# Optimization experiments

Hardware: AMD Instinct MI355X
Metric: run time of the kernel (lower is better)

## Reference

```python
import jax, jax.numpy as jnp
import numpy as np

B, L, C, NH = 4, 2048, 512, 8
HD = C // NH  # head_dim = 64


def setup_inputs() -> dict:
    key = jax.random.key(0)
    k1, k2, k3, k4 = jax.random.split(key, 4)
    s = 1.0 / np.sqrt(C)
    return {
        "x": jax.random.normal(k1, (B, L, C), dtype=jnp.float32),
        "w_qkv": jax.random.normal(k2, (C, 3 * C), dtype=jnp.float32) * s,
        "b_qkv": jnp.zeros((3 * C,), dtype=jnp.float32),  # zeroed in __init__
        "w_proj": jax.random.normal(k3, (C, C), dtype=jnp.float32) * s,
        "b_proj": jax.random.normal(k4, (C,), dtype=jnp.float32) * 0.01,
    }


def reference(x, w_qkv, b_qkv, w_proj, b_proj):
    Bx, Lx, Cx = x.shape
    qkv = x @ w_qkv + b_qkv                       # [B, L, 3C]
    qkv = qkv.reshape(Bx, Lx, 3, NH, HD)          # 'B L (K H D)'
    qkv = jnp.transpose(qkv, (2, 0, 3, 1, 4))     # 'K B H L D'
    q, k, v = qkv[0], qkv[1], qkv[2]
    scale = 1.0 / np.sqrt(HD)
    scores = jnp.einsum('bhld,bhmd->bhlm', q, k) * scale  # [B, H, L, L]
    attn = jax.nn.softmax(scores, axis=-1)
    out = jnp.einsum('bhlm,bhmd->bhld', attn, v)  # [B, H, L, D]
    out = jnp.transpose(out, (0, 2, 1, 3)).reshape(Bx, Lx, Cx)  # 'B H L D -> B L (H D)'
    return out @ w_proj + b_proj
```

## Files before the change

kernel.cpp:

```cpp
#include <hip/hip_runtime.h>

#define B_   4
#define L_   2048
#define C_   512
#define NH_  8
#define HD_  64
#define M_   (B_ * L_)
#define N_QKV 1536

typedef __bf16 bf16x8 __attribute__((ext_vector_type(8)));
typedef float floatx4 __attribute__((ext_vector_type(4)));
typedef unsigned short ushort_t;

__device__ __forceinline__ unsigned pk2(float a, float b) {
  union { float f; unsigned u; } x, y;
  x.f = a; y.f = b;
  return __builtin_amdgcn_perm(y.u + 0x8000u, x.u + 0x8000u, 0x07060302u);
}

__device__ __forceinline__ ushort_t bf16h(float a) {
  union { float f; unsigned u; } x;
  x.f = a;
  return (ushort_t)((x.u + 0x8000u) >> 16);
}

__device__ __forceinline__ floatx4 mfma16(bf16x8 a, bf16x8 b, floatx4 c) {
  return __builtin_amdgcn_mfma_f32_16x16x32_bf16(a, b, c, 0, 0, 0);
}

__device__ __forceinline__ void gld_lds16(const void* g, void* s) {
  __builtin_amdgcn_global_load_lds(
      (const __attribute__((address_space(1))) unsigned int*)(g),
      (__attribute__((address_space(3))) unsigned int*)(s), 16, 0, 0);
}

__global__ __launch_bounds__(256) void convert_all_kernel(
    const float* __restrict__ x, const float* __restrict__ wq,
    const float* __restrict__ wp, ushort_t* __restrict__ xb,
    ushort_t* __restrict__ wqT, ushort_t* __restrict__ wpT) {
  __shared__ ushort_t tile[64][68];
  const int t = threadIdx.x;
  const int bid = blockIdx.x;
  if (bid < 2048) {
    size_t i = ((size_t)bid * 256 + t) * 8;
    float4 a = *(const float4*)(x + i);
    float4 b = *(const float4*)(x + i + 4);
    uint4 o;
    o.x = pk2(a.x, a.y);
    o.y = pk2(a.z, a.w);
    o.z = pk2(b.x, b.y);
    o.w = pk2(b.z, b.w);
    *(uint4*)(xb + i) = o;
    return;
  }
  const float* w;
  ushort_t* wt;
  int N, n0, k0;
  if (bid < 2240) {
    int b2 = bid - 2048;
    w = wq; wt = wqT; N = N_QKV;
    n0 = (b2 % 24) * 64; k0 = (b2 / 24) * 64;
  } else {
    int b2 = bid - 2240;
    w = wp; wt = wpT; N = C_;
    n0 = (b2 & 7) * 64; k0 = (b2 >> 3) * 64;
  }
  const int r = t >> 4, c4 = (t & 15) * 4;
#pragma unroll
  for (int i = 0; i < 4; ++i) {
    int k = r + i * 16;
    float4 v = *(const float4*)(w + (size_t)(k0 + k) * N + n0 + c4);
    uint2 p;
    p.x = pk2(v.x, v.y);
    p.y = pk2(v.z, v.w);
    *(uint2*)&tile[k][c4] = p;
  }
  __syncthreads();
#pragma unroll
  for (int i = 0; i < 4; ++i) {
    int n = r + i * 16;
    uint2 o;
    o.x = (unsigned)tile[c4 + 0][n] | ((unsigned)tile[c4 + 1][n] << 16);
    o.y = (unsigned)tile[c4 + 2][n] | ((unsigned)tile[c4 + 3][n] << 16);
    *(uint2*)(wt + (size_t)(n0 + n) * 512 + k0 + c4) = o;
  }
}

__global__ __launch_bounds__(256) void qkv_mfma_kernel(
    const ushort_t* __restrict__ A,
    const ushort_t* __restrict__ Bt,
    const float* __restrict__ bias,
    ushort_t* __restrict__ Qd, ushort_t* __restrict__ Kd,
    ushort_t* __restrict__ Vd) {
  __shared__ ushort_t As[2][4096];
  __shared__ ushort_t Bs[2][4096];

  const int t = threadIdx.x;
  const int w = t >> 6, l = t & 63;
  const int li = l & 15, lq = l >> 4;
  const int wm = w & 1, wn = w >> 1;
  const int m0 = blockIdx.x * 128;
  const int n0 = blockIdx.y * 128;

  const int inner = (l & 7) ^ (l >> 3);
  const int srow = (l >> 3) * 2 + (inner >> 2);
  const int skb = inner & 3;

  const ushort_t* asrc0 = A + (size_t)(m0 + (2 * w) * 16 + srow) * 512 + skb * 8;
  const ushort_t* asrc1 = A + (size_t)(m0 + (2 * w + 1) * 16 + srow) * 512 + skb * 8;
  const ushort_t* bsrc0 = Bt + (size_t)(n0 + (2 * w) * 16 + srow) * 512 + skb * 8;
  const ushort_t* bsrc1 = Bt + (size_t)(n0 + (2 * w + 1) * 16 + srow) * 512 + skb * 8;
  const int qo0 = (2 * w) * 512, qo1 = (2 * w + 1) * 512;

  const int foff = (li >> 1) * 128 + ((((li & 1) * 4 + lq)) ^ (li >> 1)) * 16;

  const floatx4 fz = {0.f, 0.f, 0.f, 0.f};
  floatx4 acc[4][4];
#pragma unroll
  for (int i = 0; i < 4; ++i)
#pragma unroll
    for (int j = 0; j < 4; ++j) acc[i][j] = fz;

  for (int kk = 0; kk < 8; ++kk) {
    __syncthreads();
#pragma unroll
    for (int kh = 0; kh < 2; ++kh) {
      gld_lds16(asrc0 + kh * 32, &As[kh][qo0]);
      gld_lds16(asrc1 + kh * 32, &As[kh][qo1]);
      gld_lds16(bsrc0 + kh * 32, &Bs[kh][qo0]);
      gld_lds16(bsrc1 + kh * 32, &Bs[kh][qo1]);
    }
    asrc0 += 64; asrc1 += 64; bsrc0 += 64; bsrc1 += 64;
    __syncthreads();

#pragma unroll
    for (int kh = 0; kh < 2; ++kh) {
      bf16x8 af[4], bfr[4];
#pragma unroll
      for (int mt = 0; mt < 4; ++mt)
        af[mt] = *(const bf16x8*)((const char*)&As[kh][0] +
                                  (wm * 64 + mt * 16) * 64 + foff);
#pragma unroll
      for (int nt = 0; nt < 4; ++nt)
        bfr[nt] = *(const bf16x8*)((const char*)&Bs[kh][0] +
                                   (wn * 64 + nt * 16) * 64 + foff);
#pragma unroll
      for (int mt = 0; mt < 4; ++mt)
#pragma unroll
        for (int nt = 0; nt < 4; ++nt)
          acc[mt][nt] = mfma16(af[mt], bfr[nt], acc[mt][nt]);
    }
  }

  const int n0g = n0 + wn * 64;
  const int kk2 = n0g >> 9, h = (n0g >> 6) & 7;
  const int mb = m0 + wm * 64;
  const int b = mb >> 11;
  const int bh = b * NH_ + h;
  const float SCQ = 0.18033688011f;
  float bb[4];
#pragma unroll
  for (int nt = 0; nt < 4; ++nt) bb[nt] = bias[n0g + nt * 16 + li];

  if (kk2 == 0) {
#pragma unroll
    for (int mt = 0; mt < 4; ++mt) {
      int lrow = (mb + mt * 16 + lq * 4) & (L_ - 1);
#pragma unroll
      for (int nt = 0; nt < 4; ++nt) {
        int d = nt * 16 + li;
        ushort_t* p = Qd + ((size_t)bh * L_ + lrow) * HD_ + d;
#pragma unroll
        for (int r = 0; r < 4; ++r)
          p[(size_t)r * HD_] = bf16h((acc[mt][nt][r] + bb[nt]) * SCQ);
      }
    }
  } else if (kk2 == 1) {
#pragma unroll
    for (int mt = 0; mt < 4; ++mt) {
      int lrow = (mb + mt * 16 + lq * 4) & (L_ - 1);
#pragma unroll
      for (int nt = 0; nt < 4; ++nt) {
        int d = nt * 16 + li;
        ushort_t* p = Kd + ((size_t)bh * L_ + lrow) * HD_ + d;
#pragma unroll
        for (int r = 0; r < 4; ++r)
          p[(size_t)r * HD_] = bf16h(acc[mt][nt][r] + bb[nt]);
      }
    }
  } else {
#pragma unroll
    for (int mt = 0; mt < 4; ++mt) {
      int tb = mb + mt * 16 + lq * 4;
      int c = (tb >> 6) & 31;
      int sp = (mt >> 1) & 1;
      int rem = tb & 31;
      int lq2 = rem >> 3;
      int h8 = (rem >> 2) & 1;
#pragma unroll
      for (int nt = 0; nt < 4; ++nt) {
        size_t off = ((size_t)(bh * 32 + c) * 512 +
                      ((sp * 4 + nt) * 4 + lq2) * 16 + li) * 8 + h8 * 4;
        uint2 v;
        v.x = pk2(acc[mt][nt][0] + bb[nt], acc[mt][nt][1] + bb[nt]);
        v.y = pk2(acc[mt][nt][2] + bb[nt], acc[mt][nt][3] + bb[nt]);
        *(uint2*)(Vd + off) = v;
      }
    }
  }
}

__global__ __launch_bounds__(256) void attn_kernel(
    const ushort_t* __restrict__ Qg, const ushort_t* __restrict__ Kg,
    const ushort_t* __restrict__ Vb, ushort_t* __restrict__ AO) {
  __shared__ ushort_t Ks[4][4096];
  __shared__ ushort_t Vs[4][4096];

  const int t = threadIdx.x;
  const int w = t >> 6, l = t & 63;
  const int li = l & 15, lq = l >> 4;
  const int bh = blockIdx.y;
  const int m0 = blockIdx.x * 128;

  const ushort_t* ksrc[2];
  const ushort_t* vsrc[2];
  int qoff[2];
#pragma unroll
  for (int u = 0; u < 2; ++u) {
    int q = 2 * w + u;
    int p = q * 64 + l;
    int key = p >> 3, pb = p & 7;
    int swz = (key & 3) | (((key >> 3) & 1) << 2);
    ksrc[u] = Kg + ((size_t)bh * L_ + key) * HD_ + (pb ^ swz) * 8;
    vsrc[u] = Vb + ((size_t)bh * 32 * 512 + p) * 8;
    qoff[u] = p * 8 & 4095;
  }

  bf16x8 qf[2][2];
#pragma unroll
  for (int g = 0; g < 2; ++g)
#pragma unroll
    for (int s = 0; s < 2; ++s)
      qf[g][s] = *(const bf16x8*)(Qg +
          ((size_t)bh * L_ + m0 + (2 * w + g) * 16 + li) * HD_ + 32 * s + lq * 8);

  const floatx4 fz = {0.f, 0.f, 0.f, 0.f};
  floatx4 O[2][4];
  float lsum[2] = {0.f, 0.f};
#pragma unroll
  for (int g = 0; g < 2; ++g)
#pragma unroll
    for (int dt = 0; dt < 4; ++dt) O[g][dt] = fz;

  const int keybase = 8 * (li >> 2) + (li & 3);
  const int xsw = li & 7;

  for (int c = 0; c < L_ / 256; ++c) {
    __syncthreads();
#pragma unroll
    for (int j = 0; j < 4; ++j) {
      gld_lds16(ksrc[0] + j * 4096, &Ks[j][qoff[0]]);
      gld_lds16(ksrc[1] + j * 4096, &Ks[j][qoff[1]]);
      gld_lds16(vsrc[0] + j * 4096, &Vs[j][qoff[0]]);
      gld_lds16(vsrc[1] + j * 4096, &Vs[j][qoff[1]]);
    }
    ksrc[0] += 16384; ksrc[1] += 16384;
    vsrc[0] += 16384; vsrc[1] += 16384;
    __syncthreads();

#pragma unroll
    for (int j = 0; j < 4; ++j) {
#pragma unroll
      for (int sp = 0; sp < 2; ++sp) {
        floatx4 sa[2][2];
#pragma unroll
        for (int g = 0; g < 2; ++g)
#pragma unroll
          for (int k2 = 0; k2 < 2; ++k2) sa[g][k2] = fz;

#pragma unroll
        for (int k2 = 0; k2 < 2; ++k2) {
          const char* rowb =
              (const char*)&Ks[j][0] + (32 * sp + 4 * k2 + keybase) * 128;
#pragma unroll
          for (int s = 0; s < 2; ++s) {
            bf16x8 kf = *(const bf16x8*)(rowb + ((4 * s + lq) ^ xsw) * 16);
            sa[0][k2] = mfma16(kf, qf[0][s], sa[0][k2]);
            sa[1][k2] = mfma16(kf, qf[1][s], sa[1][k2]);
          }
        }

        bf16x8 pf[2];
#pragma unroll
        for (int g = 0; g < 2; ++g) {
          float pv[2][4];
#pragma unroll
          for (int k2 = 0; k2 < 2; ++k2)
#pragma unroll
            for (int r = 0; r < 4; ++r) {
              float e = __builtin_amdgcn_exp2f(sa[g][k2][r]);
              pv[k2][r] = e;
              lsum[g] += e;
            }
          uint4 pk;
          pk.x = pk2(pv[0][0], pv[0][1]);
          pk.y = pk2(pv[0][2], pv[0][3]);
          pk.z = pk2(pv[1][0], pv[1][1]);
          pk.w = pk2(pv[1][2], pv[1][3]);
          pf[g] = __builtin_bit_cast(bf16x8, pk);
        }

#pragma unroll
        for (int dt = 0; dt < 4; ++dt) {
          bf16x8 vf = *(const bf16x8*)((const char*)&Vs[j][0] +
              sp * 4096 + dt * 1024 + lq * 256 + li * 16);
          O[0][dt] = mfma16(vf, pf[0], O[0][dt]);
          O[1][dt] = mfma16(vf, pf[1], O[1][dt]);
        }
      }
    }
  }

  const int b = bh >> 3, h = bh & 7;
#pragma unroll
  for (int g = 0; g < 2; ++g) {
    float s = lsum[g];
    s += __shfl_xor(s, 16, 64);
    s += __shfl_xor(s, 32, 64);
    float inv = 1.0f / s;
    int qrow = m0 + (2 * w + g) * 16 + li;
    ushort_t* base = AO + ((size_t)(b * L_ + qrow)) * C_ + h * HD_ + 4 * lq;
#pragma unroll
    for (int dt = 0; dt < 4; ++dt) {
      uint2 v;
      v.x = pk2(O[g][dt][0] * inv, O[g][dt][1] * inv);
      v.y = pk2(O[g][dt][2] * inv, O[g][dt][3] * inv);
      *(uint2*)(base + 16 * dt) = v;
    }
  }
}

__global__ __launch_bounds__(256) void proj_mfma_kernel(
    const ushort_t* __restrict__ A,
    const ushort_t* __restrict__ Bt,
    const float* __restrict__ bias, float* __restrict__ out) {
  __shared__ ushort_t As[2][2048];
  __shared__ ushort_t Bs[2][4096];

  const int t = threadIdx.x;
  const int w = t >> 6, l = t & 63;
  const int li = l & 15, lq = l >> 4;
  const int wm = w & 1, wn = w >> 1;
  const int m0 = blockIdx.x * 64;
  const int n0 = blockIdx.y * 128;

  const int inner = (l & 7) ^ (l >> 3);
  const int srow = (l >> 3) * 2 + (inner >> 2);
  const int skb = inner & 3;

  const ushort_t* asrc0 = A + (size_t)(m0 + w * 16 + srow) * 512 + skb * 8;
  const ushort_t* bsrc0 = Bt + (size_t)(n0 + (2 * w) * 16 + srow) * 512 + skb * 8;
  const ushort_t* bsrc1 = Bt + (size_t)(n0 + (2 * w + 1) * 16 + srow) * 512 + skb * 8;
  const int ao = w * 512;
  const int qo0 = (2 * w) * 512, qo1 = (2 * w + 1) * 512;

  const int foff = (li >> 1) * 128 + ((((li & 1) * 4 + lq)) ^ (li >> 1)) * 16;

  const floatx4 fz = {0.f, 0.f, 0.f, 0.f};
  floatx4 acc[2][4];
#pragma unroll
  for (int i = 0; i < 2; ++i)
#pragma unroll
    for (int j = 0; j < 4; ++j) acc[i][j] = fz;

  for (int kk = 0; kk < 8; ++kk) {
    __syncthreads();
#pragma unroll
    for (int kh = 0; kh < 2; ++kh) {
      gld_lds16(asrc0 + kh * 32, &As[kh][ao]);
      gld_lds16(bsrc0 + kh * 32, &Bs[kh][qo0]);
      gld_lds16(bsrc1 + kh * 32, &Bs[kh][qo1]);
    }
    asrc0 += 64; bsrc0 += 64; bsrc1 += 64;
    __syncthreads();

#pragma unroll
    for (int kh = 0; kh < 2; ++kh) {
      bf16x8 af[2], bfr[4];
#pragma unroll
      for (int mt = 0; mt < 2; ++mt)
        af[mt] = *(const bf16x8*)((const char*)&As[kh][0] +
                                  (wm * 32 + mt * 16) * 64 + foff);
#pragma unroll
      for (int nt = 0; nt < 4; ++nt)
        bfr[nt] = *(const bf16x8*)((const char*)&Bs[kh][0] +
                                   (wn * 64 + nt * 16) * 64 + foff);
#pragma unroll
      for (int mt = 0; mt < 2; ++mt)
#pragma unroll
        for (int nt = 0; nt < 4; ++nt)
          acc[mt][nt] = mfma16(af[mt], bfr[nt], acc[mt][nt]);
    }
  }

#pragma unroll
  for (int mt = 0; mt < 2; ++mt) {
    int m = m0 + wm * 32 + mt * 16 + lq * 4;
#pragma unroll
    for (int nt = 0; nt < 4; ++nt) {
      int n = n0 + wn * 64 + nt * 16 + li;
      float bb = bias[n];
#pragma unroll
      for (int r = 0; r < 4; ++r)
        out[(size_t)(m + r) * C_ + n] = acc[mt][nt][r] + bb;
    }
  }
}

extern "C" void kernel_launch(void* const* d_in, const int* in_sizes, int n_in,
                              void* d_out, int out_size, void* d_ws,
                              size_t ws_size, hipStream_t stream) {
  const float* x      = (const float*)d_in[0];
  const float* w_qkv  = (const float*)d_in[1];
  const float* b_qkv  = (const float*)d_in[2];
  const float* w_proj = (const float*)d_in[3];
  const float* b_proj = (const float*)d_in[4];
  float* out = (float*)d_out;

  ushort_t* ws     = (ushort_t*)d_ws;
  ushort_t* Qd     = ws;
  ushort_t* Kd     = ws + 4194304;
  ushort_t* Vd     = ws + 8388608;
  ushort_t* AO     = ws + 12582912;
  ushort_t* xb     = ws + 16777216;
  ushort_t* wqkvT  = ws + 20971520;
  ushort_t* wprojT = ws + 21757952;

  convert_all_kernel<<<2304, 256, 0, stream>>>(x, w_qkv, w_proj, xb, wqkvT,
                                               wprojT);

  dim3 g1(M_ / 128, N_QKV / 128);
  qkv_mfma_kernel<<<g1, 256, 0, stream>>>(xb, wqkvT, b_qkv, Qd, Kd, Vd);

  dim3 g2(L_ / 128, B_ * NH_);
  attn_kernel<<<g2, 256, 0, stream>>>(Qd, Kd, Vd, AO);

  dim3 g3(M_ / 64, C_ / 128);
  proj_mfma_kernel<<<g3, 256, 0, stream>>>(AO, wprojT, b_proj, out);
}
```

Baseline: 155.3 us.

## Shrink attention tiles to 64 query rows and 128-key chunks for more blocks

The attention kernel now gives each wave 16 query rows instead of 32, so a block covers 64 queries, and it stages 128 keys per iteration instead of 256, halving LDS use. The grid becomes 1024 one-dimensional blocks with the head index in the low bits, which raises occupancy and groups blocks of the same query range across heads. In exchange K/V tiles are reused across half as many queries, so global/L2 traffic for K and V doubles and there are twice as many barriers per block.

```diff
diff --git a/kernel.cpp b/kernel.cpp
--- a/kernel.cpp
+++ b/kernel.cpp
@@ -213,14 +213,14 @@
 __global__ __launch_bounds__(256) void attn_kernel(
     const ushort_t* __restrict__ Qg, const ushort_t* __restrict__ Kg,
     const ushort_t* __restrict__ Vb, ushort_t* __restrict__ AO) {
-  __shared__ ushort_t Ks[4][4096];
-  __shared__ ushort_t Vs[4][4096];
+  __shared__ ushort_t Ks[2][4096];
+  __shared__ ushort_t Vs[2][4096];
 
   const int t = threadIdx.x;
   const int w = t >> 6, l = t & 63;
   const int li = l & 15, lq = l >> 4;
-  const int bh = blockIdx.y;
-  const int m0 = blockIdx.x * 128;
+  const int bh = blockIdx.x & 31;
+  const int m0 = (blockIdx.x >> 5) * 64;
 
   const ushort_t* ksrc[2];
   const ushort_t* vsrc[2];
@@ -233,50 +233,44 @@
     int swz = (key & 3) | (((key >> 3) & 1) << 2);
     ksrc[u] = Kg + ((size_t)bh * L_ + key) * HD_ + (pb ^ swz) * 8;
     vsrc[u] = Vb + ((size_t)bh * 32 * 512 + p) * 8;
-    qoff[u] = p * 8 & 4095;
-  }
-
-  bf16x8 qf[2][2];
-#pragma unroll
-  for (int g = 0; g < 2; ++g)
-#pragma unroll
-    for (int s = 0; s < 2; ++s)
-      qf[g][s] = *(const bf16x8*)(Qg +
-          ((size_t)bh * L_ + m0 + (2 * w + g) * 16 + li) * HD_ + 32 * s + lq * 8);
+    qoff[u] = p * 8;
+  }
+
+  bf16x8 qf[2];
+#pragma unroll
+  for (int s = 0; s < 2; ++s)
+    qf[s] = *(const bf16x8*)(Qg +
+        ((size_t)bh * L_ + m0 + w * 16 + li) * HD_ + 32 * s + lq * 8);
 
   const floatx4 fz = {0.f, 0.f, 0.f, 0.f};
-  floatx4 O[2][4];
-  float lsum[2] = {0.f, 0.f};
-#pragma unroll
-  for (int g = 0; g < 2; ++g)
-#pragma unroll
-    for (int dt = 0; dt < 4; ++dt) O[g][dt] = fz;
+  floatx4 O[4];
+  float lsum = 0.f;
+#pragma unroll
+  for (int dt = 0; dt < 4; ++dt) O[dt] = fz;
 
   const int keybase = 8 * (li >> 2) + (li & 3);
   const int xsw = li & 7;
 
-  for (int c = 0; c < L_ / 256; ++c) {
-    __syncthreads();
-#pragma unroll
-    for (int j = 0; j < 4; ++j) {
+  for (int c = 0; c < L_ / 128; ++c) {
+    __syncthreads();
+#pragma unroll
+    for (int j = 0; j < 2; ++j) {
       gld_lds16(ksrc[0] + j * 4096, &Ks[j][qoff[0]]);
       gld_lds16(ksrc[1] + j * 4096, &Ks[j][qoff[1]]);
       gld_lds16(vsrc[0] + j * 4096, &Vs[j][qoff[0]]);
       gld_lds16(vsrc[1] + j * 4096, &Vs[j][qoff[1]]);
     }
-    ksrc[0] += 16384; ksrc[1] += 16384;
-    vsrc[0] += 16384; vsrc[1] += 16384;
-    __syncthreads();
-
-#pragma unroll
-    for (int j = 0; j < 4; ++j) {
+    ksrc[0] += 8192; ksrc[1] += 8192;
+    vsrc[0] += 8192; vsrc[1] += 8192;
+    __syncthreads();
+
+#pragma unroll
+    for (int j = 0; j < 2; ++j) {
 #pragma unroll
       for (int sp = 0; sp < 2; ++sp) {
-        floatx4 sa[2][2];
-#pragma unroll
-        for (int g = 0; g < 2; ++g)
-#pragma unroll
-          for (int k2 = 0; k2 < 2; ++k2) sa[g][k2] = fz;
+        floatx4 sa[2];
+#pragma unroll
+        for (int k2 = 0; k2 < 2; ++k2) sa[k2] = fz;
 
 #pragma unroll
         for (int k2 = 0; k2 < 2; ++k2) {
@@ -285,58 +279,49 @@
 #pragma unroll
           for (int s = 0; s < 2; ++s) {
             bf16x8 kf = *(const bf16x8*)(rowb + ((4 * s + lq) ^ xsw) * 16);
-            sa[0][k2] = mfma16(kf, qf[0][s], sa[0][k2]);
-            sa[1][k2] = mfma16(kf, qf[1][s], sa[1][k2]);
+            sa[k2] = mfma16(kf, qf[s], sa[k2]);
           }
         }
 
-        bf16x8 pf[2];
-#pragma unroll
-        for (int g = 0; g < 2; ++g) {
-          float pv[2][4];
-#pragma unroll
-          for (int k2 = 0; k2 < 2; ++k2)
-#pragma unroll
-            for (int r = 0; r < 4; ++r) {
-              float e = __builtin_amdgcn_exp2f(sa[g][k2][r]);
-              pv[k2][r] = e;
-              lsum[g] += e;
-            }
-          uint4 pk;
-          pk.x = pk2(pv[0][0], pv[0][1]);
-          pk.y = pk2(pv[0][2], pv[0][3]);
-          pk.z = pk2(pv[1][0], pv[1][1]);
-          pk.w = pk2(pv[1][2], pv[1][3]);
-          pf[g] = __builtin_bit_cast(bf16x8, pk);
-        }
+        float pv[2][4];
+#pragma unroll
+        for (int k2 = 0; k2 < 2; ++k2)
+#pragma unroll
+          for (int r = 0; r < 4; ++r) {
+            float e = __builtin_amdgcn_exp2f(sa[k2][r]);
+            pv[k2][r] = e;
+            lsum += e;
+          }
+        uint4 pk;
+        pk.x = pk2(pv[0][0], pv[0][1]);
+        pk.y = pk2(pv[0][2], pv[0][3]);
+        pk.z = pk2(pv[1][0], pv[1][1]);
+        pk.w = pk2(pv[1][2], pv[1][3]);
+        bf16x8 pf = __builtin_bit_cast(bf16x8, pk);
 
 #pragma unroll
         for (int dt = 0; dt < 4; ++dt) {
           bf16x8 vf = *(const bf16x8*)((const char*)&Vs[j][0] +
               sp * 4096 + dt * 1024 + lq * 256 + li * 16);
-          O[0][dt] = mfma16(vf, pf[0], O[0][dt]);
-          O[1][dt] = mfma16(vf, pf[1], O[1][dt]);
+          O[dt] = mfma16(vf, pf, O[dt]);
         }
       }
     }
   }
 
   const int b = bh >> 3, h = bh & 7;
-#pragma unroll
-  for (int g = 0; g < 2; ++g) {
-    float s = lsum[g];
-    s += __shfl_xor(s, 16, 64);
-    s += __shfl_xor(s, 32, 64);
-    float inv = 1.0f / s;
-    int qrow = m0 + (2 * w + g) * 16 + li;
-    ushort_t* base = AO + ((size_t)(b * L_ + qrow)) * C_ + h * HD_ + 4 * lq;
-#pragma unroll
-    for (int dt = 0; dt < 4; ++dt) {
-      uint2 v;
-      v.x = pk2(O[g][dt][0] * inv, O[g][dt][1] * inv);
-      v.y = pk2(O[g][dt][2] * inv, O[g][dt][3] * inv);
-      *(uint2*)(base + 16 * dt) = v;
-    }
+  float s = lsum;
+  s += __shfl_xor(s, 16, 64);
+  s += __shfl_xor(s, 32, 64);
+  float inv = 1.0f / s;
+  int qrow = m0 + w * 16 + li;
+  ushort_t* base = AO + ((size_t)(b * L_ + qrow)) * C_ + h * HD_ + 4 * lq;
+#pragma unroll
+  for (int dt = 0; dt < 4; ++dt) {
+    uint2 v;
+    v.x = pk2(O[dt][0] * inv, O[dt][1] * inv);
+    v.y = pk2(O[dt][2] * inv, O[dt][3] * inv);
+    *(uint2*)(base + 16 * dt) = v;
   }
 }
 
@@ -442,8 +427,7 @@
   dim3 g1(M_ / 128, N_QKV / 128);
   qkv_mfma_kernel<<<g1, 256, 0, stream>>>(xb, wqkvT, b_qkv, Qd, Kd, Vd);
 
-  dim3 g2(L_ / 128, B_ * NH_);
-  attn_kernel<<<g2, 256, 0, stream>>>(Qd, Kd, Vd, AO);
+  attn_kernel<<<1024, 256, 0, stream>>>(Qd, Kd, Vd, AO);
 
   dim3 g3(M_ / 64, C_ / 128);
   proj_mfma_kernel<<<g3, 256, 0, stream>>>(AO, wprojT, b_proj, out);
```

Result: slower. 158.5 us (+2.1%).

## Split attention keys across two wave groups and shrink GEMM tiles for occupancy

Applied to the files above, without the earlier changes.

The attention kernel now runs 512-thread blocks in which two groups of four waves each process half of the key sequence for the same 128 queries. Their partial outputs and row sums are combined through shared memory at the end, and the block index is remapped so each block covers one head and one query tile. Both the QKV and projection GEMMs move to 64-wide N tiles, so each wave holds fewer accumulators and more blocks are launched. The aim is more parallelism and better CU fill, paid for with an extra LDS reduction and less operand reuse per block in the GEMMs.

```diff
diff --git a/kernel.cpp b/kernel.cpp
--- a/kernel.cpp
+++ b/kernel.cpp
@@ -93,14 +93,13 @@
     ushort_t* __restrict__ Qd, ushort_t* __restrict__ Kd,
     ushort_t* __restrict__ Vd) {
   __shared__ ushort_t As[2][4096];
-  __shared__ ushort_t Bs[2][4096];
+  __shared__ ushort_t Bs[2][2048];
 
   const int t = threadIdx.x;
   const int w = t >> 6, l = t & 63;
   const int li = l & 15, lq = l >> 4;
-  const int wm = w & 1, wn = w >> 1;
   const int m0 = blockIdx.x * 128;
-  const int n0 = blockIdx.y * 128;
+  const int n0 = blockIdx.y * 64;
 
   const int inner = (l & 7) ^ (l >> 3);
   const int srow = (l >> 3) * 2 + (inner >> 2);
@@ -108,16 +107,16 @@
 
   const ushort_t* asrc0 = A + (size_t)(m0 + (2 * w) * 16 + srow) * 512 + skb * 8;
   const ushort_t* asrc1 = A + (size_t)(m0 + (2 * w + 1) * 16 + srow) * 512 + skb * 8;
-  const ushort_t* bsrc0 = Bt + (size_t)(n0 + (2 * w) * 16 + srow) * 512 + skb * 8;
-  const ushort_t* bsrc1 = Bt + (size_t)(n0 + (2 * w + 1) * 16 + srow) * 512 + skb * 8;
+  const ushort_t* bsrc0 = Bt + (size_t)(n0 + w * 16 + srow) * 512 + skb * 8;
   const int qo0 = (2 * w) * 512, qo1 = (2 * w + 1) * 512;
+  const int bo0 = w * 512;
 
   const int foff = (li >> 1) * 128 + ((((li & 1) * 4 + lq)) ^ (li >> 1)) * 16;
 
   const floatx4 fz = {0.f, 0.f, 0.f, 0.f};
-  floatx4 acc[4][4];
-#pragma unroll
-  for (int i = 0; i < 4; ++i)
+  floatx4 acc[2][4];
+#pragma unroll
+  for (int i = 0; i < 2; ++i)
 #pragma unroll
     for (int j = 0; j < 4; ++j) acc[i][j] = fz;
 
@@ -127,44 +126,42 @@
     for (int kh = 0; kh < 2; ++kh) {
       gld_lds16(asrc0 + kh * 32, &As[kh][qo0]);
       gld_lds16(asrc1 + kh * 32, &As[kh][qo1]);
-      gld_lds16(bsrc0 + kh * 32, &Bs[kh][qo0]);
-      gld_lds16(bsrc1 + kh * 32, &Bs[kh][qo1]);
-    }
-    asrc0 += 64; asrc1 += 64; bsrc0 += 64; bsrc1 += 64;
+      gld_lds16(bsrc0 + kh * 32, &Bs[kh][bo0]);
+    }
+    asrc0 += 64; asrc1 += 64; bsrc0 += 64;
     __syncthreads();
 
 #pragma unroll
     for (int kh = 0; kh < 2; ++kh) {
-      bf16x8 af[4], bfr[4];
-#pragma unroll
-      for (int mt = 0; mt < 4; ++mt)
+      bf16x8 af[2], bfr[4];
+#pragma unroll
+      for (int mt = 0; mt < 2; ++mt)
         af[mt] = *(const bf16x8*)((const char*)&As[kh][0] +
-                                  (wm * 64 + mt * 16) * 64 + foff);
+                                  (w * 32 + mt * 16) * 64 + foff);
 #pragma unroll
       for (int nt = 0; nt < 4; ++nt)
         bfr[nt] = *(const bf16x8*)((const char*)&Bs[kh][0] +
-                                   (wn * 64 + nt * 16) * 64 + foff);
-#pragma unroll
-      for (int mt = 0; mt < 4; ++mt)
+                                   (nt * 16) * 64 + foff);
+#pragma unroll
+      for (int mt = 0; mt < 2; ++mt)
 #pragma unroll
         for (int nt = 0; nt < 4; ++nt)
           acc[mt][nt] = mfma16(af[mt], bfr[nt], acc[mt][nt]);
     }
   }
 
-  const int n0g = n0 + wn * 64;
-  const int kk2 = n0g >> 9, h = (n0g >> 6) & 7;
-  const int mb = m0 + wm * 64;
-  const int b = mb >> 11;
+  const int kk2 = n0 >> 9, h = (n0 >> 6) & 7;
+  const int mb = m0 + w * 32;
+  const int b = m0 >> 11;
   const int bh = b * NH_ + h;
   const float SCQ = 0.18033688011f;
   float bb[4];
 #pragma unroll
-  for (int nt = 0; nt < 4; ++nt) bb[nt] = bias[n0g + nt * 16 + li];
+  for (int nt = 0; nt < 4; ++nt) bb[nt] = bias[n0 + nt * 16 + li];
 
   if (kk2 == 0) {
 #pragma unroll
-    for (int mt = 0; mt < 4; ++mt) {
+    for (int mt = 0; mt < 2; ++mt) {
       int lrow = (mb + mt * 16 + lq * 4) & (L_ - 1);
 #pragma unroll
       for (int nt = 0; nt < 4; ++nt) {
@@ -177,7 +174,7 @@
     }
   } else if (kk2 == 1) {
 #pragma unroll
-    for (int mt = 0; mt < 4; ++mt) {
+    for (int mt = 0; mt < 2; ++mt) {
       int lrow = (mb + mt * 16 + lq * 4) & (L_ - 1);
 #pragma unroll
       for (int nt = 0; nt < 4; ++nt) {
@@ -190,11 +187,12 @@
     }
   } else {
 #pragma unroll
-    for (int mt = 0; mt < 4; ++mt) {
+    for (int mt = 0; mt < 2; ++mt) {
       int tb = mb + mt * 16 + lq * 4;
+      int key = tb & 63;
       int c = (tb >> 6) & 31;
-      int sp = (mt >> 1) & 1;
-      int rem = tb & 31;
+      int sp = key >> 5;
+      int rem = key & 31;
       int lq2 = rem >> 3;
       int h8 = (rem >> 2) & 1;
 #pragma unroll
@@ -210,30 +208,36 @@
   }
 }
 
-__global__ __launch_bounds__(256) void attn_kernel(
+__global__ __launch_bounds__(512) void attn_kernel(
     const ushort_t* __restrict__ Qg, const ushort_t* __restrict__ Kg,
     const ushort_t* __restrict__ Vb, ushort_t* __restrict__ AO) {
-  __shared__ ushort_t Ks[4][4096];
-  __shared__ ushort_t Vs[4][4096];
+  __shared__ __align__(16) char smem[35328];
+  ushort_t* KsB = (ushort_t*)smem;
+  ushort_t* VsB = (ushort_t*)(smem + 16384);
+  float* Oc = (float*)smem;
+  float* Lc = (float*)(smem + 34816);
 
   const int t = threadIdx.x;
   const int w = t >> 6, l = t & 63;
+  const int g2 = w >> 2, wl = w & 3;
   const int li = l & 15, lq = l >> 4;
-  const int bh = blockIdx.y;
-  const int m0 = blockIdx.x * 128;
+  const int bh = blockIdx.x & 31;
+  const int m0 = (blockIdx.x >> 5) * 128;
+
+  ushort_t* Ks = KsB + g2 * 4096;
+  ushort_t* Vs = VsB + g2 * 4096;
 
   const ushort_t* ksrc[2];
   const ushort_t* vsrc[2];
-  int qoff[2];
+  int koff[2];
 #pragma unroll
   for (int u = 0; u < 2; ++u) {
-    int q = 2 * w + u;
-    int p = q * 64 + l;
+    int p = (2 * wl + u) * 64 + l;
     int key = p >> 3, pb = p & 7;
     int swz = (key & 3) | (((key >> 3) & 1) << 2);
-    ksrc[u] = Kg + ((size_t)bh * L_ + key) * HD_ + (pb ^ swz) * 8;
-    vsrc[u] = Vb + ((size_t)bh * 32 * 512 + p) * 8;
-    qoff[u] = p * 8 & 4095;
+    ksrc[u] = Kg + ((size_t)bh * L_ + g2 * 1024 + key) * HD_ + (pb ^ swz) * 8;
+    vsrc[u] = Vb + ((size_t)bh * 32 * 512 + (size_t)g2 * 16 * 512 + p) * 8;
+    koff[u] = p * 8;
   }
 
   bf16x8 qf[2][2];
@@ -242,7 +246,7 @@
 #pragma unroll
     for (int s = 0; s < 2; ++s)
       qf[g][s] = *(const bf16x8*)(Qg +
-          ((size_t)bh * L_ + m0 + (2 * w + g) * 16 + li) * HD_ + 32 * s + lq * 8);
+          ((size_t)bh * L_ + m0 + wl * 32 + 16 * g + li) * HD_ + 32 * s + lq * 8);
 
   const floatx4 fz = {0.f, 0.f, 0.f, 0.f};
   floatx4 O[2][4];
@@ -255,87 +259,106 @@
   const int keybase = 8 * (li >> 2) + (li & 3);
   const int xsw = li & 7;
 
-  for (int c = 0; c < L_ / 256; ++c) {
-    __syncthreads();
-#pragma unroll
-    for (int j = 0; j < 4; ++j) {
-      gld_lds16(ksrc[0] + j * 4096, &Ks[j][qoff[0]]);
-      gld_lds16(ksrc[1] + j * 4096, &Ks[j][qoff[1]]);
-      gld_lds16(vsrc[0] + j * 4096, &Vs[j][qoff[0]]);
-      gld_lds16(vsrc[1] + j * 4096, &Vs[j][qoff[1]]);
-    }
-    ksrc[0] += 16384; ksrc[1] += 16384;
-    vsrc[0] += 16384; vsrc[1] += 16384;
-    __syncthreads();
-
-#pragma unroll
-    for (int j = 0; j < 4; ++j) {
-#pragma unroll
-      for (int sp = 0; sp < 2; ++sp) {
-        floatx4 sa[2][2];
-#pragma unroll
-        for (int g = 0; g < 2; ++g)
-#pragma unroll
-          for (int k2 = 0; k2 < 2; ++k2) sa[g][k2] = fz;
-
-#pragma unroll
-        for (int k2 = 0; k2 < 2; ++k2) {
-          const char* rowb =
-              (const char*)&Ks[j][0] + (32 * sp + 4 * k2 + keybase) * 128;
-#pragma unroll
-          for (int s = 0; s < 2; ++s) {
-            bf16x8 kf = *(const bf16x8*)(rowb + ((4 * s + lq) ^ xsw) * 16);
-            sa[0][k2] = mfma16(kf, qf[0][s], sa[0][k2]);
-            sa[1][k2] = mfma16(kf, qf[1][s], sa[1][k2]);
+  for (int c = 0; c < 16; ++c) {
+    __syncthreads();
+#pragma unroll
+    for (int u = 0; u < 2; ++u) {
+      gld_lds16(ksrc[u], Ks + koff[u]);
+      gld_lds16(vsrc[u], Vs + koff[u]);
+      ksrc[u] += 64 * HD_;
+      vsrc[u] += 4096;
+    }
+    __syncthreads();
+
+#pragma unroll
+    for (int sp = 0; sp < 2; ++sp) {
+      floatx4 sa[2][2];
+#pragma unroll
+      for (int g = 0; g < 2; ++g)
+#pragma unroll
+        for (int k2 = 0; k2 < 2; ++k2) sa[g][k2] = fz;
+
+#pragma unroll
+      for (int k2 = 0; k2 < 2; ++k2) {
+        const char* rowb =
+            (const char*)Ks + (32 * sp + 4 * k2 + keybase) * 128;
+#pragma unroll
+        for (int s = 0; s < 2; ++s) {
+          bf16x8 kf = *(const bf16x8*)(rowb + ((4 * s + lq) ^ xsw) * 16);
+          sa[0][k2] = mfma16(kf, qf[0][s], sa[0][k2]);
+          sa[1][k2] = mfma16(kf, qf[1][s], sa[1][k2]);
+        }
+      }
+
+      bf16x8 pf[2];
+#pragma unroll
+      for (int g = 0; g < 2; ++g) {
+        float pv[2][4];
+#pragma unroll
+        for (int k2 = 0; k2 < 2; ++k2)
+#pragma unroll
+          for (int r = 0; r < 4; ++r) {
+            float e = __builtin_amdgcn_exp2f(sa[g][k2][r]);
+            pv[k2][r] = e;
+            lsum[g] += e;
           }
-        }
-
-        bf16x8 pf[2];
-#pragma unroll
-        for (int g = 0; g < 2; ++g) {
-          float pv[2][4];
-#pragma unroll
-          for (int k2 = 0; k2 < 2; ++k2)
-#pragma unroll
-            for (int r = 0; r < 4; ++r) {
-              float e = __builtin_amdgcn_exp2f(sa[g][k2][r]);
-              pv[k2][r] = e;
-              lsum[g] += e;
-            }
-          uint4 pk;
-          pk.x = pk2(pv[0][0], pv[0][1]);
-          pk.y = pk2(pv[0][2], pv[0][3]);
-          pk.z = pk2(pv[1][0], pv[1][1]);
-          pk.w = pk2(pv[1][2], pv[1][3]);
-          pf[g] = __builtin_bit_cast(bf16x8, pk);
-        }
-
-#pragma unroll
-        for (int dt = 0; dt < 4; ++dt) {
-          bf16x8 vf = *(const bf16x8*)((const char*)&Vs[j][0] +
-              sp * 4096 + dt * 1024 + lq * 256 + li * 16);
-          O[0][dt] = mfma16(vf, pf[0], O[0][dt]);
-          O[1][dt] = mfma16(vf, pf[1], O[1][dt]);
-        }
-      }
-    }
-  }
-
-  const int b = bh >> 3, h = bh & 7;
+        uint4 pk;
+        pk.x = pk2(pv[0][0], pv[0][1]);
+        pk.y = pk2(pv[0][2], pv[0][3]);
+        pk.z = pk2(pv[1][0], pv[1][1]);
+        pk.w = pk2(pv[1][2], pv[1][3]);
+        pf[g] = __builtin_bit_cast(bf16x8, pk);
+      }
+
+#pragma unroll
+      for (int dt = 0; dt < 4; ++dt) {
+        bf16x8 vf = *(const bf16x8*)((const char*)Vs +
+            sp * 4096 + dt * 1024 + lq * 256 + li * 16);
+        O[0][dt] = mfma16(vf, pf[0], O[0][dt]);
+        O[1][dt] = mfma16(vf, pf[1], O[1][dt]);
+      }
+    }
+  }
+
+  float srow[2];
 #pragma unroll
   for (int g = 0; g < 2; ++g) {
     float s = lsum[g];
     s += __shfl_xor(s, 16, 64);
     s += __shfl_xor(s, 32, 64);
-    float inv = 1.0f / s;
-    int qrow = m0 + (2 * w + g) * 16 + li;
-    ushort_t* base = AO + ((size_t)(b * L_ + qrow)) * C_ + h * HD_ + 4 * lq;
-#pragma unroll
-    for (int dt = 0; dt < 4; ++dt) {
-      uint2 v;
-      v.x = pk2(O[g][dt][0] * inv, O[g][dt][1] * inv);
-      v.y = pk2(O[g][dt][2] * inv, O[g][dt][3] * inv);
-      *(uint2*)(base + 16 * dt) = v;
+    srow[g] = s;
+  }
+
+  __syncthreads();
+  if (g2 == 1) {
+#pragma unroll
+    for (int g = 0; g < 2; ++g) {
+      int row = wl * 32 + 16 * g + li;
+#pragma unroll
+      for (int dt = 0; dt < 4; ++dt)
+        *(floatx4*)&Oc[row * 68 + 16 * dt + 4 * lq] = O[g][dt];
+      Lc[row] = srow[g];
+    }
+  }
+  __syncthreads();
+
+  if (g2 == 0) {
+    const int b = bh >> 3, h = bh & 7;
+#pragma unroll
+    for (int g = 0; g < 2; ++g) {
+      int row = wl * 32 + 16 * g + li;
+      float inv = 1.0f / (srow[g] + Lc[row]);
+      int qrow = m0 + row;
+      ushort_t* base = AO + ((size_t)(b * L_ + qrow)) * C_ + h * HD_ + 4 * lq;
+#pragma unroll
+      for (int dt = 0; dt < 4; ++dt) {
+        floatx4 oc = *(const floatx4*)&Oc[row * 68 + 16 * dt + 4 * lq];
+        floatx4 ot = O[g][dt] + oc;
+        uint2 v;
+        v.x = pk2(ot[0] * inv, ot[1] * inv);
+        v.y = pk2(ot[2] * inv, ot[3] * inv);
+        *(uint2*)(base + 16 * dt) = v;
+      }
     }
   }
 }
@@ -345,75 +368,61 @@
     const ushort_t* __restrict__ Bt,
     const float* __restrict__ bias, float* __restrict__ out) {
   __shared__ ushort_t As[2][2048];
-  __shared__ ushort_t Bs[2][4096];
+  __shared__ ushort_t Bs[2][2048];
 
   const int t = threadIdx.x;
   const int w = t >> 6, l = t & 63;
   const int li = l & 15, lq = l >> 4;
-  const int wm = w & 1, wn = w >> 1;
   const int m0 = blockIdx.x * 64;
-  const int n0 = blockIdx.y * 128;
+  const int n0 = blockIdx.y * 64;
 
   const int inner = (l & 7) ^ (l >> 3);
   const int srow = (l >> 3) * 2 + (inner >> 2);
   const int skb = inner & 3;
 
   const ushort_t* asrc0 = A + (size_t)(m0 + w * 16 + srow) * 512 + skb * 8;
-  const ushort_t* bsrc0 = Bt + (size_t)(n0 + (2 * w) * 16 + srow) * 512 + skb * 8;
-  const ushort_t* bsrc1 = Bt + (size_t)(n0 + (2 * w + 1) * 16 + srow) * 512 + skb * 8;
-  const int ao = w * 512;
-  const int qo0 = (2 * w) * 512, qo1 = (2 * w + 1) * 512;
+  const ushort_t* bsrc0 = Bt + (size_t)(n0 + w * 16 + srow) * 512 + skb * 8;
+  const int qo0 = w * 512;
 
   const int foff = (li >> 1) * 128 + ((((li & 1) * 4 + lq)) ^ (li >> 1)) * 16;
 
   const floatx4 fz = {0.f, 0.f, 0.f, 0.f};
-  floatx4 acc[2][4];
-#pragma unroll
-  for (int i = 0; i < 2; ++i)
-#pragma unroll
-    for (int j = 0; j < 4; ++j) acc[i][j] = fz;
+  floatx4 acc[4];
+#pragma unroll
+  for (int j = 0; j < 4; ++j) acc[j] = fz;
 
   for (int kk = 0; kk < 8; ++kk) {
     __syncthreads();
 #pragma unroll
     for (int kh = 0; kh < 2; ++kh) {
-      gld_lds16(asrc0 + kh * 32, &As[kh][ao]);
+      gld_lds16(asrc0 + kh * 32, &As[kh][qo0]);
       gld_lds16(bsrc0 + kh * 32, &Bs[kh][qo0]);
-      gld_lds16(bsrc1 + kh * 32, &Bs[kh][qo1]);
-    }
-    asrc0 += 64; bsrc0 += 64; bsrc1 += 64;
+    }
+    asrc0 += 64; bsrc0 += 64;
     __syncthreads();
 
 #pragma unroll
     for (int kh = 0; kh < 2; ++kh) {
-      bf16x8 af[2], bfr[4];
-#pragma unroll
-      for (int mt = 0; mt < 2; ++mt)
-        af[mt] = *(const bf16x8*)((const char*)&As[kh][0] +
-                                  (wm * 32 + mt * 16) * 64 + foff);
+      bf16x8 af, bfr[4];
+      af = *(const bf16x8*)((const char*)&As[kh][0] + (w * 16) * 64 + foff);
 #pragma unroll
       for (int nt = 0; nt < 4; ++nt)
         bfr[nt] = *(const bf16x8*)((const char*)&Bs[kh][0] +
-                                   (wn * 64 + nt * 16) * 64 + foff);
-#pragma unroll
-      for (int mt = 0; mt < 2; ++mt)
-#pragma unroll
-        for (int nt = 0; nt < 4; ++nt)
-          acc[mt][nt] = mfma16(af[mt], bfr[nt], acc[mt][nt]);
-    }
-  }
-
-#pragma unroll
-  for (int mt = 0; mt < 2; ++mt) {
-    int m = m0 + wm * 32 + mt * 16 + lq * 4;
-#pragma unroll
-    for (int nt = 0; nt < 4; ++nt) {
-      int n = n0 + wn * 64 + nt * 16 + li;
-      float bb = bias[n];
-#pragma unroll
-      for (int r = 0; r < 4; ++r)
-        out[(size_t)(m + r) * C_ + n] = acc[mt][nt][r] + bb;
-    }
+                                   (nt * 16) * 64 + foff);
+#pragma unroll
+      for (int nt = 0; nt < 4; ++nt)
+        acc[nt] = mfma16(af, bfr[nt], acc[nt]);
+    }
+  }
+
+  const int m = m0 + w * 16 + lq * 4;
+#pragma unroll
+  for (int nt = 0; nt < 4; ++nt) {
+    int n = n0 + nt * 16 + li;
+    float bb = bias[n];
+#pragma unroll
+    for (int r = 0; r < 4; ++r)
+      out[(size_t)(m + r) * C_ + n] = acc[nt][r] + bb;
   }
 }
 
@@ -439,12 +448,11 @@
   convert_all_kernel<<<2304, 256, 0, stream>>>(x, w_qkv, w_proj, xb, wqkvT,
                                                wprojT);
 
-  dim3 g1(M_ / 128, N_QKV / 128);
+  dim3 g1(M_ / 128, N_QKV / 64);
   qkv_mfma_kernel<<<g1, 256, 0, stream>>>(xb, wqkvT, b_qkv, Qd, Kd, Vd);
 
-  dim3 g2(L_ / 128, B_ * NH_);
-  attn_kernel<<<g2, 256, 0, stream>>>(Qd, Kd, Vd, AO);
-
-  dim3 g3(M_ / 64, C_ / 128);
+  attn_kernel<<<512, 512, 0, stream>>>(Qd, Kd, Vd, AO);
+
+  dim3 g3(M_ / 64, C_ / 64);
   proj_mfma_kernel<<<g3, 256, 0, stream>>>(AO, wprojT, b_proj, out);
 }
```

After: 148.5 us. 4.3% less time.
